# Optimization experiments

Measured on AMD Instinct MI355X. Metric: run time of the kernel, lower is better.

Reference implementation:

```python
import jax, jax.numpy as jnp
import numpy as np

B, N, D = 8, 2048, 768
H = 12
HD = D // H
W = 16          # window_size
HOP = 8         # hop_size
GB = N // 2 + 1   # global freq bins = 1025
LB = W // 2 + 1   # local freq bins = 9
NW = (N - W) // HOP + 1  # num windows = 255
EPS_LN = 1e-5


def setup_inputs() -> dict:
    key = jax.random.key(0)
    ks = jax.random.split(key, 12)
    s = 0.02
    return {
        "x": jax.random.normal(ks[0], (B, N, D), dtype=jnp.float32),
        "base_filter_global": jnp.ones((H, GB, 1), jnp.float32),
        "base_filter_local": jnp.ones((H, LB, 1), jnp.float32),
        "modrelu_bias_global": jnp.full((H, GB, 1), -0.1, jnp.float32),
        "modrelu_bias_local": jnp.full((H, LB, 1), -0.1, jnp.float32),
        "w1g": jax.random.normal(ks[1], (D, D), jnp.float32) * s,
        "b1g": jnp.zeros((D,), jnp.float32),
        "w2g": jax.random.normal(ks[2], (D, H * GB), jnp.float32) * s,
        "b2g": jnp.zeros((H * GB,), jnp.float32),
        "w1l": jax.random.normal(ks[3], (D, D), jnp.float32) * s,
        "b1l": jnp.zeros((D,), jnp.float32),
        "w2l": jax.random.normal(ks[4], (D, H * LB), jnp.float32) * s,
        "b2l": jnp.zeros((H * LB,), jnp.float32),
        "fusion_w": jax.random.normal(ks[5], (2,), jnp.float32) * 0.5,
        "ln_gamma": jnp.ones((D,), jnp.float32),
        "ln_beta": jnp.zeros((D,), jnp.float32),
    }


def _modrelu(z, bias):
    # modReLU: ReLU(|z| + b) * z / |z|  (|z| clamped at 1e-6 in denominator)
    a = jnp.abs(z)
    return z * (jax.nn.relu(a + bias) / jnp.maximum(a, 1e-6))


def _hann(w):
    # torch.hann_window default (periodic=True)
    n = jnp.arange(w, dtype=jnp.float32)
    return 0.5 * (1.0 - jnp.cos(2.0 * jnp.pi * n / w))


def reference(x, base_filter_global, base_filter_local, modrelu_bias_global,
              modrelu_bias_local, w1g, b1g, w2g, b2g, w1l, b1l, w2l, b2l,
              fusion_w, ln_gamma, ln_beta):
    b, n, d = x.shape
    x_heads = x.reshape(b, n, H, HD).transpose(0, 2, 1, 3)  # (B,H,N,hd)

    # ---- global branch ----
    Fg = jnp.fft.rfft(x_heads, axis=2, norm='ortho')  # (B,H,GB,hd) complex
    ctx = x.mean(axis=1)  # (B,D)
    mg = jnp.tanh(jax.nn.gelu(ctx @ w1g + b1g, approximate=False) @ w2g + b2g)
    mg = mg.reshape(b, H, GB, 1)
    Fg = Fg * (base_filter_global[None] + mg)
    Fg = _modrelu(Fg, modrelu_bias_global[None])
    x_global = jnp.fft.irfft(Fg, n=n, axis=2, norm='ortho')  # (B,H,N,hd)

    # ---- local (STFT) branch ----
    idx = jnp.arange(NW)[:, None] * HOP + jnp.arange(W)[None, :]  # (NW,W)
    x_win = x_heads[:, :, idx, :]  # (B,H,NW,W,hd)
    w = _hann(W)[None, None, None, :, None]
    x_win = x_win * w
    Fl = jnp.fft.rfft(x_win, axis=3, norm='ortho')  # (B,H,NW,LB,hd)
    ml = jnp.tanh(jax.nn.gelu(ctx @ w1l + b1l, approximate=False) @ w2l + b2l)
    ml = ml.reshape(b, H, 1, LB, 1)
    Fl = Fl * (base_filter_local[None, :, None] + ml)
    Fl = _modrelu(Fl, modrelu_bias_local[None, :, None])
    x_lwin = jnp.fft.irfft(Fl, n=W, axis=3, norm='ortho') * w  # (B,H,NW,W,hd)

    # vectorized overlap-add
    flat_idx = idx.reshape(-1)  # (NW*W,)
    x_local = jnp.zeros((b, H, n, HD), x.dtype).at[:, :, flat_idx, :].add(
        x_lwin.reshape(b, H, NW * W, HD))

    # ---- fuse + residual + layernorm ----
    fused = x_global * fusion_w[0] + x_local * fusion_w[1]  # Linear(2,1,bias=False)
    x_out = fused.transpose(0, 2, 1, 3).reshape(b, n, d)
    y = x + x_out  # dropout is identity at p=0 / eval
    mu = y.mean(axis=-1, keepdims=True)
    var = y.var(axis=-1, keepdims=True)
    return (y - mu) / jnp.sqrt(var + EPS_LN) * ln_gamma + ln_beta
```

## Files before the change

### kernel.cpp

```cpp
#include <hip/hip_runtime.h>
#include <math.h>

#define B_  8
#define N_  2048
#define D_  768
#define H_  12
#define HD_ 64
#define GB_ 1025
#define LB_ 9
#define NW_ 255

#define CBX(i) ((i) + ((i) >> 4))

#define C1_ 0.92387953251128674f
#define S1_ 0.38268343236508978f
#define R2_ 0.70710678118654752f

#define FBF(i,k,wr,wi) { const float ar=yr[i],ai=yi[i],br=yr[k],bi=yi[k]; \
  yr[i]=ar+br; yi[i]=ai+bi; const float dr=ar-br, di=ai-bi; \
  yr[k]=fmaf(dr,wr,-(di*(wi))); yi[k]=fmaf(dr,wi,di*(wr)); }
#define FBF1(i,k) { const float ar=yr[i],ai=yi[i],br=yr[k],bi=yi[k]; \
  yr[i]=ar+br; yi[i]=ai+bi; yr[k]=ar-br; yi[k]=ai-bi; }
#define FBFmi(i,k) { const float ar=yr[i],ai=yi[i],br=yr[k],bi=yi[k]; \
  yr[i]=ar+br; yi[i]=ai+bi; yr[k]=ai-bi; yi[k]=br-ar; }

#define IBF(i,k,wr,wi) { const float br=yr[k],bi=yi[k]; \
  const float tr=fmaf(br,wr,-(bi*(wi))), ti=fmaf(br,wi,bi*(wr)); \
  yr[k]=yr[i]-tr; yi[k]=yi[i]-ti; yr[i]+=tr; yi[i]+=ti; }
#define IBF1(i,k) { const float tr=yr[k], ti=yi[k]; \
  yr[k]=yr[i]-tr; yi[k]=yi[i]-ti; yr[i]+=tr; yi[i]+=ti; }
#define IBFpi(i,k) { const float tr=-yi[k], ti=yr[k]; \
  yr[k]=yr[i]-tr; yi[k]=yi[i]-ti; yr[i]+=tr; yi[i]+=ti; }

__device__ __forceinline__ float2 cmulf(float2 a, float2 b) {
  return make_float2(fmaf(a.x, b.x, -(a.y*b.y)), fmaf(a.x, b.y, a.y*b.x));
}
__device__ __forceinline__ float2 caddf(float2 a, float2 b){ return make_float2(a.x+b.x, a.y+b.y); }
__device__ __forceinline__ float2 csubf(float2 a, float2 b){ return make_float2(a.x-b.x, a.y-b.y); }

__global__ __launch_bounds__(256) void k_ctx(const float* __restrict__ x,
                                             float* __restrict__ ctx) {
  const int b = blockIdx.x;
  const int nc = blockIdx.y;
  const int tid = threadIdx.x;
  const int n0 = nc * 64;
  for (int c = tid; c < D_; c += 256) {
    float s = 0.0f;
    #pragma unroll 4
    for (int n = 0; n < 64; ++n)
      s += x[((size_t)(b*N_ + n0 + n))*D_ + c];
    atomicAdd(&ctx[b*D_ + c], s);
  }
}

__global__ __launch_bounds__(256) void k_mlp1(
    const float* __restrict__ ctx,
    const float* __restrict__ w1g, const float* __restrict__ b1g,
    const float* __restrict__ w1l, const float* __restrict__ b1l,
    float* __restrict__ h1g, float* __restrict__ h1l) {
  __shared__ float hs[B_*D_];
  __shared__ float red[4][16][33];
  const int tid = threadIdx.x;
  const bool isl = (blockIdx.y != 0);
  const float* w1 = isl ? w1l : w1g;
  const float* b1 = isl ? b1l : b1g;
  float*       h1 = isl ? h1l : h1g;
  const int j0 = (int)blockIdx.x * 64;

  for (int i = tid; i < B_*D_; i += 256) hs[i] = ctx[i] * (1.0f/(float)N_);
  __syncthreads();

  const int jg    = tid & 15;
  const int slice = tid >> 4;
  const int j     = j0 + jg*4;
  float acc[8][4] = {};
  {
    const float4* w14 = (const float4*)w1;
    const int jc = j >> 2;
    const int i0 = slice*48;
    #pragma unroll 4
    for (int ii = 0; ii < 48; ++ii) {
      const int i = i0 + ii;
      const float4 w = w14[(size_t)i*192 + jc];
      #pragma unroll
      for (int b = 0; b < 8; ++b) {
        const float hv = hs[b*D_ + i];
        acc[b][0] = fmaf(hv, w.x, acc[b][0]);
        acc[b][1] = fmaf(hv, w.y, acc[b][1]);
        acc[b][2] = fmaf(hv, w.z, acc[b][2]);
        acc[b][3] = fmaf(hv, w.w, acc[b][3]);
      }
    }
  }
  #pragma unroll
  for (int b = 0; b < 8; ++b) {
    #pragma unroll
    for (int q = 0; q < 4; ++q) {
      float v = acc[b][q];
      v += __shfl_xor(v, 16, 64);
      v += __shfl_xor(v, 32, 64);
      acc[b][q] = v;
    }
  }
  const int wv = tid >> 6;
  if ((tid & 63) < 16) {
    #pragma unroll
    for (int b = 0; b < 8; ++b)
      #pragma unroll
      for (int q = 0; q < 4; ++q)
        red[wv][jg][b*4+q] = acc[b][q];
  }
  __syncthreads();
  for (int s = tid; s < 512; s += 256) {
    const int jg2 = s >> 5;
    const int v2  = s & 31;
    const int b   = v2 >> 2, q = v2 & 3;
    const int jo  = j0 + jg2*4 + q;
    const float sum = red[0][jg2][v2] + red[1][jg2][v2]
                    + red[2][jg2][v2] + red[3][jg2][v2];
    const float v = sum + b1[jo];
    h1[(size_t)b*D_ + jo] = 0.5f * v * (1.0f + erff(v * 0.70710678118654752f));
  }
}

__global__ __launch_bounds__(256) void k_mlp2(
    const float* __restrict__ h1g, const float* __restrict__ h1l,
    const float* __restrict__ w2g, const float* __restrict__ b2g,
    const float* __restrict__ w2l, const float* __restrict__ b2l,
    float* __restrict__ mg, float* __restrict__ ml) {
  __shared__ float hs[B_*D_];
  __shared__ float red[4][16][33];
  const int tid = threadIdx.x;
  const bool isg = (blockIdx.x < 193);
  const float* h1 = isg ? h1g : h1l;
  const float* w2 = isg ? w2g : w2l;
  const float* b2 = isg ? b2g : b2l;
  float*       mo = isg ? mg  : ml;
  const int Jmax = isg ? (H_*GB_) : (H_*LB_);
  const int j0   = isg ? (int)blockIdx.x*64 : ((int)blockIdx.x-193)*64;

  for (int i = tid; i < B_*D_; i += 256) hs[i] = h1[i];
  __syncthreads();

  const int jg    = tid & 15;
  const int slice = tid >> 4;
  const int j     = j0 + jg*4;
  float acc[8][4] = {};
  if (j < Jmax) {
    const float4* w24 = (const float4*)w2;
    const int jc   = j >> 2;
    const int rowq = Jmax >> 2;
    const int i0   = slice*48;
    #pragma unroll 4
    for (int ii = 0; ii < 48; ++ii) {
      const int i = i0 + ii;
      const float4 w = w24[(size_t)i*rowq + jc];
      #pragma unroll
      for (int b = 0; b < 8; ++b) {
        const float hv = hs[b*D_ + i];
        acc[b][0] = fmaf(hv, w.x, acc[b][0]);
        acc[b][1] = fmaf(hv, w.y, acc[b][1]);
        acc[b][2] = fmaf(hv, w.z, acc[b][2]);
        acc[b][3] = fmaf(hv, w.w, acc[b][3]);
      }
    }
  }
  #pragma unroll
  for (int b = 0; b < 8; ++b) {
    #pragma unroll
    for (int q = 0; q < 4; ++q) {
      float v = acc[b][q];
      v += __shfl_xor(v, 16, 64);
      v += __shfl_xor(v, 32, 64);
      acc[b][q] = v;
    }
  }
  const int wv = tid >> 6;
  if ((tid & 63) < 16) {
    #pragma unroll
    for (int b = 0; b < 8; ++b)
      #pragma unroll
      for (int q = 0; q < 4; ++q)
        red[wv][jg][b*4+q] = acc[b][q];
  }
  __syncthreads();
  for (int s = tid; s < 512; s += 256) {
    const int jg2 = s >> 5;
    const int v2  = s & 31;
    const int b   = v2 >> 2, q = v2 & 3;
    const int jo  = j0 + jg2*4 + q;
    if (jo < Jmax) {
      const float sum = red[0][jg2][v2] + red[1][jg2][v2]
                      + red[2][jg2][v2] + red[3][jg2][v2];
      mo[(size_t)b*Jmax + jo] = tanhf(sum + b2[jo]);
    }
  }
}

__global__ __launch_bounds__(256) void k_spectral(
    const float* __restrict__ x,
    const float* __restrict__ bfg, const float* __restrict__ bfl,
    const float* __restrict__ mbg, const float* __restrict__ mbl,
    const float* __restrict__ mg,  const float* __restrict__ ml,
    const float* __restrict__ fw,  float* __restrict__ fused) {
  __shared__ float2 cb[N_ + (N_>>4)];
  __shared__ float2 tw[1024];
  __shared__ float  t1b[4][8], t2b[4][8];
  __shared__ float  lf[LB_], lb[LB_];

  const int tid = threadIdx.x;
  const int id  = blockIdx.x;
  const int v_  = (id & 7) * 384 + (id >> 3);
  const int dp  = v_ & 31;
  const int bh  = v_ >> 5;
  const int h   = bh % H_;
  const int b   = bh / H_;
  const int d   = dp * 2;
  const int c   = h*HD_ + d;
  const int col0 = bh*HD_ + d;

  for (int m = tid; m < 1024; m += 256) {
    float s_, c_;
    sincospif(-(float)m * (1.0f/1024.0f), &s_, &c_);
    tw[m] = make_float2(c_, s_);
  }
  if (tid < LB_) {
    lf[tid] = bfl[h*LB_ + tid] + ml[(size_t)b*(H_*LB_) + h*LB_ + tid];
    lb[tid] = mbl[h*LB_ + tid];
  }
  for (int n = tid; n < N_; n += 256) {
    const float2 v = *(const float2*)&x[((size_t)(b*N_ + n))*D_ + c];
    cb[CBX(n)] = v;
  }
  __syncthreads();

  const float HWIN[16] = {0.0f, 0.038060233744356624f, 0.14644660940672624f, 0.30865828381745508f,
                          0.5f, 0.69134171618254492f, 0.85355339059327376f, 0.96193976625564337f,
                          1.0f, 0.96193976625564337f, 0.85355339059327376f, 0.69134171618254492f,
                          0.5f, 0.30865828381745508f, 0.14644660940672624f, 0.038060233744356624f};
  float w1a[16], w2a[16];
  {
    const int j = tid;
    if (j < NW_) {
      float yr[16], yi[16];
      #pragma unroll
      for (int t = 0; t < 16; ++t) {
        const float2 v = cb[CBX(j*8 + t)];
        yr[t] = v.x * HWIN[t];
        yi[t] = v.y * HWIN[t];
      }
      FBF1(0,8); FBF(1,9,C1_,-S1_); FBF(2,10,R2_,-R2_); FBF(3,11,S1_,-C1_);
      FBFmi(4,12); FBF(5,13,-S1_,-C1_); FBF(6,14,-R2_,-R2_); FBF(7,15,-C1_,-S1_);
      FBF1(0,4); FBF(1,5,R2_,-R2_); FBFmi(2,6); FBF(3,7,-R2_,-R2_);
      FBF1(8,12); FBF(9,13,R2_,-R2_); FBFmi(10,14); FBF(11,15,-R2_,-R2_);
      FBF1(0,2); FBFmi(1,3); FBF1(4,6); FBFmi(5,7);
      FBF1(8,10); FBFmi(9,11); FBF1(12,14); FBFmi(13,15);
      FBF1(0,1); FBF1(2,3); FBF1(4,5); FBF1(6,7);
      FBF1(8,9); FBF1(10,11); FBF1(12,13); FBF1(14,15);
      {
        const int IA[9] = {0,8,4,12,2,10,6,14,1};
        const int IB[9] = {0,15,7,11,3,13,5,9,1};
        #pragma unroll
        for (int l = 0; l <= 8; ++l) {
          const int ia = IA[l], ib = IB[l];
          const float Zar=yr[ia], Zai=yi[ia], Zbr=yr[ib], Zbi=yi[ib];
          float f1r = 0.125f*(Zar+Zbr), f1i = 0.125f*(Zai-Zbi);
          float f2r = 0.125f*(Zai+Zbi), f2i = 0.125f*(Zbr-Zar);
          const float ft = lf[l], bs = lb[l];
          f1r *= ft; f1i *= ft; f2r *= ft; f2i *= ft;
          const float a1 = sqrtf(f1r*f1r + f1i*f1i);
          const float m1 = fmaxf(a1 + bs, 0.0f) / fmaxf(a1, 1e-6f);
          f1r *= m1; f1i *= m1;
          const float a2 = sqrtf(f2r*f2r + f2i*f2i);
          const float m2 = fmaxf(a2 + bs, 0.0f) / fmaxf(a2, 1e-6f);
          f2r *= m2; f2i *= m2;
          yr[ia] = f1r - f2i; yi[ia] = f1i + f2r;
          if (l >= 1 && l <= 7) { yr[ib] = f1r + f2i; yi[ib] = f2r - f1i; }
        }
      }
      IBF1(0,1); IBF1(2,3); IBF1(4,5); IBF1(6,7);
      IBF1(8,9); IBF1(10,11); IBF1(12,13); IBF1(14,15);
      IBF1(0,2); IBFpi(1,3); IBF1(4,6); IBFpi(5,7);
      IBF1(8,10); IBFpi(9,11); IBF1(12,14); IBFpi(13,15);
      IBF1(0,4); IBF(1,5,R2_,R2_); IBFpi(2,6); IBF(3,7,-R2_,R2_);
      IBF1(8,12); IBF(9,13,R2_,R2_); IBFpi(10,14); IBF(11,15,-R2_,R2_);
      IBF1(0,8); IBF(1,9,C1_,S1_); IBF(2,10,R2_,R2_); IBF(3,11,S1_,C1_);
      IBFpi(4,12); IBF(5,13,-S1_,C1_); IBF(6,14,-R2_,R2_); IBF(7,15,-C1_,S1_);
      #pragma unroll
      for (int t = 0; t < 16; ++t) {
        const float q = 0.25f * HWIN[t];
        w1a[t] = yr[t] * q;
        w2a[t] = yi[t] * q;
      }
    } else {
      #pragma unroll
      for (int t = 0; t < 16; ++t) { w1a[t] = 0.0f; w2a[t] = 0.0f; }
    }
  }
  const int lane = tid & 63, wvi = tid >> 6;
  if (lane == 63 && tid < NW_) {
    #pragma unroll
    for (int s = 0; s < 8; ++s) { t1b[wvi][s] = w1a[8+s]; t2b[wvi][s] = w2a[8+s]; }
  }
  __syncthreads();

  float r1[8], r2[8];
  #pragma unroll
  for (int s = 0; s < 8; ++s) {
    float p1 = __shfl_up(w1a[s+8], 1, 64);
    float p2 = __shfl_up(w2a[s+8], 1, 64);
    if (lane == 0) {
      p1 = wvi ? t1b[wvi-1][s] : 0.0f;
      p2 = wvi ? t2b[wvi-1][s] : 0.0f;
    }
    r1[s] = w1a[s] + p1;
    r2[s] = w2a[s] + p2;
  }

  #pragma unroll
  for (int sh = 10; sh >= 2; sh -= 2) {
    const int hspan = 1 << sh, hh = hspan >> 1;
    for (int t = tid; t < 512; t += 256) {
      const int p  = t & (hh-1);
      const int g  = t >> (sh-1);
      const int i0 = (g << (sh+1)) | p;
      float2 a = cb[CBX(i0)], bb = cb[CBX(i0+hh)], cc = cb[CBX(i0+hspan)], dd = cb[CBX(i0+hspan+hh)];
      const float2 w1  = tw[p << (10-sh)];
      const float2 w1b = tw[(p+hh) << (10-sh)];
      const float2 w2  = tw[p << (11-sh)];
      float2 ap = caddf(a, cc),  cp = cmulf(csubf(a, cc), w1);
      float2 bp = caddf(bb, dd), dp2 = cmulf(csubf(bb, dd), w1b);
      cb[CBX(i0)]          = caddf(ap, bp);
      cb[CBX(i0+hh)]       = cmulf(csubf(ap, bp), w2);
      cb[CBX(i0+hspan)]    = caddf(cp, dp2);
      cb[CBX(i0+hspan+hh)] = cmulf(csubf(cp, dp2), w2);
    }
    __syncthreads();
  }
  for (int t = tid; t < 1024; t += 256) {
    const int i0 = t << 1;
    float2 a = cb[CBX(i0)], bb = cb[CBX(i0+1)];
    cb[CBX(i0)]   = caddf(a, bb);
    cb[CBX(i0+1)] = csubf(a, bb);
  }
  __syncthreads();

  const float fsc = 0.022097086912079610f;
  {
    const float* mgp = mg + (size_t)b*(H_*GB_) + h*GB_;
    const float* bfp = bfg + h*GB_;
    const float* mbp = mbg + h*GB_;
    for (int k = tid; k < 1024; k += 256) {
      if (k == 0) {
        float2 Z0 = cb[CBX(0)], Zn = cb[CBX(1)];
        float g1 = Z0.x * fsc, g2 = Z0.y * fsc;
        {
          const float filt = bfp[0] + mgp[0], bias = mbp[0];
          g1 *= filt; g2 *= filt;
          float a1 = fabsf(g1); g1 *= fmaxf(a1 + bias, 0.0f) / fmaxf(a1, 1e-6f);
          float a2 = fabsf(g2); g2 *= fmaxf(a2 + bias, 0.0f) / fmaxf(a2, 1e-6f);
        }
        cb[CBX(0)] = make_float2(g1, g2);
        float n1 = Zn.x * fsc, n2 = Zn.y * fsc;
        {
          const float filt = bfp[1024] + mgp[1024], bias = mbp[1024];
          n1 *= filt; n2 *= filt;
          float a1 = fabsf(n1); n1 *= fmaxf(a1 + bias, 0.0f) / fmaxf(a1, 1e-6f);
          float a2 = fabsf(n2); n2 *= fmaxf(a2 + bias, 0.0f) / fmaxf(a2, 1e-6f);
        }
        cb[CBX(1)] = make_float2(n1, n2);
      } else {
        const int ik  = (int)(__brev((unsigned)k) >> 21);
        const int imk = (int)(__brev((unsigned)(2048 - k)) >> 21);
        const float2 Za = cb[CBX(ik)], Zb = cb[CBX(imk)];
        const float hs_ = 0.5f * fsc;
        float f1r = (Za.x + Zb.x) * hs_, f1i = (Za.y - Zb.y) * hs_;
        float f2r = (Za.y + Zb.y) * hs_, f2i = (Zb.x - Za.x) * hs_;
        const float filt = bfp[k] + mgp[k], bias = mbp[k];
        f1r *= filt; f1i *= filt; f2r *= filt; f2i *= filt;
        const float a1 = sqrtf(f1r*f1r + f1i*f1i);
        const float s1 = fmaxf(a1 + bias, 0.0f) / fmaxf(a1, 1e-6f);
        f1r *= s1; f1i *= s1;
        const float a2 = sqrtf(f2r*f2r + f2i*f2i);
        const float s2 = fmaxf(a2 + bias, 0.0f) / fmaxf(a2, 1e-6f);
        f2r *= s2; f2i *= s2;
        cb[CBX(ik)]  = make_float2(f1r - f2i, f1i + f2r);
        cb[CBX(imk)] = make_float2(f1r + f2i, f2r - f1i);
      }
    }
  }
  __syncthreads();

  for (int t = tid; t < 1024; t += 256) {
    const int i0 = t << 1;
    float2 a = cb[CBX(i0)], bb = cb[CBX(i0+1)];
    cb[CBX(i0)]   = caddf(a, bb);
    cb[CBX(i0+1)] = csubf(a, bb);
  }
  __syncthreads();
  #pragma unroll
  for (int sh = 2; sh <= 10; sh += 2) {
    const int hspan = 1 << sh, hh = hspan >> 1;
    for (int t = tid; t < 512; t += 256) {
      const int p  = t & (hh-1);
      const int g  = t >> (sh-1);
      const int i0 = (g << (sh+1)) | p;
      float2 a = cb[CBX(i0)], bb = cb[CBX(i0+hh)], cc = cb[CBX(i0+hspan)], dd = cb[CBX(i0+hspan+hh)];
      float2 w2  = tw[p << (11-sh)];       w2.y  = -w2.y;
      float2 w1  = tw[p << (10-sh)];       w1.y  = -w1.y;
      float2 w1b = tw[(p+hh) << (10-sh)];  w1b.y = -w1b.y;
      float2 t1 = cmulf(bb, w2);
      float2 ap = caddf(a, t1),  bp = csubf(a, t1);
      float2 t2 = cmulf(dd, w2);
      float2 cp = caddf(cc, t2), dp2 = csubf(cc, t2);
      float2 T = cmulf(cp, w1);
      float2 U = cmulf(dp2, w1b);
      cb[CBX(i0)]          = caddf(ap, T);
      cb[CBX(i0+hspan)]    = csubf(ap, T);
      cb[CBX(i0+hh)]       = caddf(bp, U);
      cb[CBX(i0+hspan+hh)] = csubf(bp, U);
    }
    __syncthreads();
  }

  const float fw1v = fw[1];
  const float fwg  = fw[0] * fsc;
  float* f0 = fused + (size_t)col0 * N_;
  float* f1p = f0 + N_;
  const int n0 = tid * 8;
  float v0[8], v1[8];
  #pragma unroll
  for (int s = 0; s < 8; ++s) {
    const float2 g = cb[CBX(n0 + s)];
    v0[s] = fwg * g.x + fw1v * r1[s];
    v1[s] = fwg * g.y + fw1v * r2[s];
  }
  *(float4*)&f0[n0]    = make_float4(v0[0], v0[1], v0[2], v0[3]);
  *(float4*)&f0[n0+4]  = make_float4(v0[4], v0[5], v0[6], v0[7]);
  *(float4*)&f1p[n0]   = make_float4(v1[0], v1[1], v1[2], v1[3]);
  *(float4*)&f1p[n0+4] = make_float4(v1[4], v1[5], v1[6], v1[7]);
}

__global__ __launch_bounds__(256) void k_ln(const float* __restrict__ x,
                                            const float* __restrict__ fused,
                                            const float* __restrict__ gamma,
                                            const float* __restrict__ beta,
                                            float* __restrict__ out) {
  __shared__ float yt[16*776];
  __shared__ float mus[16], rsd[16];
  const int bi = blockIdx.x;
  const int b  = bi >> 7;
  const int n0 = (bi & 127) * 16;
  const int tid = threadIdx.x;

  {
    const float4* x4 = (const float4*)(x + ((size_t)(b*N_ + n0))*D_);
    for (int i = tid; i < 16*D_/4; i += 256) {
      const int nn = i / 192, r = i - nn*192;
      const float4 v = x4[i];
      float* yp = &yt[nn*776 + r*4];
      yp[0] = v.x; yp[1] = v.y; yp[2] = v.z; yp[3] = v.w;
    }
  }
  __syncthreads();
  {
    const float4* fu4 = (const float4*)fused;
    for (int i = tid; i < 16*D_/4; i += 256) {
      const int cc = i >> 2, q = (i & 3) * 4;
      const float4 g = fu4[(((size_t)(b*D_ + cc))*N_ + n0)/4 + (i & 3)];
      yt[(q+0)*776 + cc] += g.x;
      yt[(q+1)*776 + cc] += g.y;
      yt[(q+2)*776 + cc] += g.z;
      yt[(q+3)*776 + cc] += g.w;
    }
  }
  __syncthreads();
  const int nn = tid >> 4, cl = tid & 15;
  float s1 = 0.0f, s2 = 0.0f;
  for (int c = cl; c < D_; c += 16) {
    const float v = yt[nn*776 + c];
    s1 += v; s2 += v*v;
  }
  #pragma unroll
  for (int m = 8; m >= 1; m >>= 1) {
    s1 += __shfl_xor(s1, m, 16);
    s2 += __shfl_xor(s2, m, 16);
  }
  if (cl == 0) {
    const float mu  = s1 * (1.0f/(float)D_);
    const float var = s2 * (1.0f/(float)D_) - mu*mu;
    mus[nn] = mu;
    rsd[nn] = rsqrtf(var + 1e-5f);
  }
  __syncthreads();
  {
    float4* o4 = (float4*)(out + ((size_t)(b*N_ + n0))*D_);
    const float4* g4 = (const float4*)gamma;
    const float4* be4 = (const float4*)beta;
    for (int i = tid; i < 16*D_/4; i += 256) {
      const int nn2 = i / 192, r = i - nn2*192;
      const float mu = mus[nn2], rs = rsd[nn2];
      const float4 gm = g4[r], bt = be4[r];
      const float* yp = &yt[nn2*776 + r*4];
      float4 o;
      o.x = (yp[0] - mu) * rs * gm.x + bt.x;
      o.y = (yp[1] - mu) * rs * gm.y + bt.y;
      o.z = (yp[2] - mu) * rs * gm.z + bt.z;
      o.w = (yp[3] - mu) * rs * gm.w + bt.w;
      o4[i] = o;
    }
  }
}

extern "C" void kernel_launch(void* const* d_in, const int* in_sizes, int n_in,
                              void* d_out, int out_size, void* d_ws, size_t ws_size,
                              hipStream_t stream) {
  const float* x   = (const float*)d_in[0];
  const float* bfg = (const float*)d_in[1];
  const float* bfl = (const float*)d_in[2];
  const float* mbg = (const float*)d_in[3];
  const float* mbl = (const float*)d_in[4];
  const float* w1g = (const float*)d_in[5];
  const float* b1g = (const float*)d_in[6];
  const float* w2g = (const float*)d_in[7];
  const float* b2g = (const float*)d_in[8];
  const float* w1l = (const float*)d_in[9];
  const float* b1l = (const float*)d_in[10];
  const float* w2l = (const float*)d_in[11];
  const float* b2l = (const float*)d_in[12];
  const float* fw  = (const float*)d_in[13];
  const float* gam = (const float*)d_in[14];
  const float* bet = (const float*)d_in[15];
  float* out = (float*)d_out;

  float* ws    = (float*)d_ws;
  float* ctx   = ws;
  float* h1g   = ws + 6144;
  float* h1l   = ws + 12288;
  float* mg    = ws + 18432;
  float* ml    = ws + 116832;
  float* fused = ws + 117696;

  hipMemsetAsync(ctx, 0, (size_t)B_*D_*sizeof(float), stream);
  k_ctx<<<dim3(B_, 32), 256, 0, stream>>>(x, ctx);
  k_mlp1<<<dim3(12, 2), 256, 0, stream>>>(ctx, w1g, b1g, w1l, b1l, h1g, h1l);
  k_mlp2<<<195, 256, 0, stream>>>(h1g, h1l, w2g, b2g, w2l, b2l, mg, ml);
  k_spectral<<<B_*H_*32, 256, 0, stream>>>(x, bfg, bfl, mbg, mbl, mg, ml, fw, fused);
  k_ln<<<B_*N_/16, 256, 0, stream>>>(x, fused, gam, bet, out);
}
```

Before: 312.2 us.

## Restructure 2048-point shared-memory FFT into radix-8 passes with derived twiddles

Replaces the radix-4 plus final radix-2 shared-memory FFT (six passes, each followed by a barrier, both forward and inverse) with four radix-8-style passes of 8 points per thread. Higher-power twiddles are derived in registers by squaring the base twiddle, so the twiddle table shrinks from 1024 to 256 padded entries and fewer sincos calls are needed. This aims to cut LDS round-trips and __syncthreads barriers. The cost is more registers per thread and a small extra rounding error from the squared twiddles.

```diff
diff --git a/kernel.cpp b/kernel.cpp
--- a/kernel.cpp
+++ b/kernel.cpp
@@ -11,6 +11,7 @@
 #define NW_ 255
 
 #define CBX(i) ((i) + ((i) >> 4))
+#define TWX(i) ((i) + ((i) >> 4))
 
 #define C1_ 0.92387953251128674f
 #define S1_ 0.38268343236508978f
@@ -35,8 +36,133 @@
 __device__ __forceinline__ float2 cmulf(float2 a, float2 b) {
   return make_float2(fmaf(a.x, b.x, -(a.y*b.y)), fmaf(a.x, b.y, a.y*b.x));
 }
+__device__ __forceinline__ float2 cmulcf(float2 a, float2 b) {
+  return make_float2(fmaf(a.x, b.x, a.y*b.y), fmaf(a.y, b.x, -(a.x*b.y)));
+}
 __device__ __forceinline__ float2 caddf(float2 a, float2 b){ return make_float2(a.x+b.x, a.y+b.y); }
 __device__ __forceinline__ float2 csubf(float2 a, float2 b){ return make_float2(a.x-b.x, a.y-b.y); }
+__device__ __forceinline__ float2 csqf(float2 a){ return make_float2(fmaf(a.x,a.x,-(a.y*a.y)), 2.0f*a.x*a.y); }
+
+template<int S, int L>
+__device__ __forceinline__ void fft_trip_fwd(float2* cb, const float2* tw, int j) {
+  const int r    = j & (S-1);
+  const int base = r + ((j >> L) << (L+3));
+  float2 v[8];
+  #pragma unroll
+  for (int k = 0; k < 8; ++k) v[k] = cb[CBX(base + S*k)];
+  const float2 w = tw[TWX(r * (256/S))];
+  const float2 c8 = make_float2(R2_, -R2_);
+  float2 W1[4];
+  W1[0] = w;
+  W1[1] = cmulf(w, c8);
+  W1[2] = make_float2(w.y, -w.x);
+  W1[3] = make_float2(W1[1].y, -W1[1].x);
+  #pragma unroll
+  for (int k = 0; k < 4; ++k) {
+    const float2 u = v[k], t = v[k+4];
+    v[k]   = caddf(u, t);
+    v[k+4] = cmulf(csubf(u, t), W1[k]);
+  }
+  const float2 w2  = csqf(w);
+  const float2 w2i = make_float2(w2.y, -w2.x);
+  {
+    float2 d;
+    d = csubf(v[0], v[2]); v[0] = caddf(v[0], v[2]); v[2] = cmulf(d, w2);
+    d = csubf(v[1], v[3]); v[1] = caddf(v[1], v[3]); v[3] = cmulf(d, w2i);
+    d = csubf(v[4], v[6]); v[4] = caddf(v[4], v[6]); v[6] = cmulf(d, w2);
+    d = csubf(v[5], v[7]); v[5] = caddf(v[5], v[7]); v[7] = cmulf(d, w2i);
+  }
+  const float2 w4 = csqf(w2);
+  #pragma unroll
+  for (int k = 0; k < 8; k += 2) {
+    const float2 d = csubf(v[k], v[k+1]);
+    v[k]   = caddf(v[k], v[k+1]);
+    v[k+1] = cmulf(d, w4);
+  }
+  #pragma unroll
+  for (int k = 0; k < 8; ++k) cb[CBX(base + S*k)] = v[k];
+}
+
+__device__ __forceinline__ void fft_trip4_fwd(float2* cb, int j) {
+  const int base = j << 3;
+  float2 v[8];
+  #pragma unroll
+  for (int k = 0; k < 8; ++k) v[k] = cb[CBX(base + k)];
+  float2 d;
+  d = csubf(v[0], v[2]); v[0] = caddf(v[0], v[2]); v[2] = d;
+  d = csubf(v[1], v[3]); v[1] = caddf(v[1], v[3]); v[3] = make_float2(d.y, -d.x);
+  d = csubf(v[4], v[6]); v[4] = caddf(v[4], v[6]); v[6] = d;
+  d = csubf(v[5], v[7]); v[5] = caddf(v[5], v[7]); v[7] = make_float2(d.y, -d.x);
+  #pragma unroll
+  for (int k = 0; k < 8; k += 2) {
+    d = csubf(v[k], v[k+1]);
+    v[k]   = caddf(v[k], v[k+1]);
+    v[k+1] = d;
+  }
+  #pragma unroll
+  for (int k = 0; k < 8; ++k) cb[CBX(base + k)] = v[k];
+}
+
+__device__ __forceinline__ void fft_trip1_inv(float2* cb, int j) {
+  const int base = j << 3;
+  float2 v[8];
+  #pragma unroll
+  for (int k = 0; k < 8; ++k) v[k] = cb[CBX(base + k)];
+  #pragma unroll
+  for (int k = 0; k < 8; k += 2) {
+    const float2 t = v[k+1];
+    v[k+1] = csubf(v[k], t);
+    v[k]   = caddf(v[k], t);
+  }
+  {
+    float2 t;
+    t = v[2];                              v[2] = csubf(v[0], t); v[0] = caddf(v[0], t);
+    t = make_float2(-v[3].y, v[3].x);      v[3] = csubf(v[1], t); v[1] = caddf(v[1], t);
+    t = v[6];                              v[6] = csubf(v[4], t); v[4] = caddf(v[4], t);
+    t = make_float2(-v[7].y, v[7].x);      v[7] = csubf(v[5], t); v[5] = caddf(v[5], t);
+  }
+  #pragma unroll
+  for (int k = 0; k < 8; ++k) cb[CBX(base + k)] = v[k];
+}
+
+template<int S, int L>
+__device__ __forceinline__ void fft_trip_inv(float2* cb, const float2* tw, int j) {
+  const int r    = j & (S-1);
+  const int base = r + ((j >> L) << (L+3));
+  float2 v[8];
+  #pragma unroll
+  for (int k = 0; k < 8; ++k) v[k] = cb[CBX(base + S*k)];
+  const float2 w  = tw[TWX(r * (256/S))];
+  const float2 w2 = csqf(w);
+  const float2 w4 = csqf(w2);
+  #pragma unroll
+  for (int k = 0; k < 8; k += 2) {
+    const float2 t = cmulcf(v[k+1], w4);
+    v[k+1] = csubf(v[k], t);
+    v[k]   = caddf(v[k], t);
+  }
+  {
+    float2 t;
+    t = cmulcf(v[2], w2);                          v[2] = csubf(v[0], t); v[0] = caddf(v[0], t);
+    t = cmulcf(v[3], w2); t = make_float2(-t.y, t.x); v[3] = csubf(v[1], t); v[1] = caddf(v[1], t);
+    t = cmulcf(v[6], w2);                          v[6] = csubf(v[4], t); v[4] = caddf(v[4], t);
+    t = cmulcf(v[7], w2); t = make_float2(-t.y, t.x); v[7] = csubf(v[5], t); v[5] = caddf(v[5], t);
+  }
+  const float2 c8 = make_float2(R2_, -R2_);
+  float2 W1[4];
+  W1[0] = w;
+  W1[1] = cmulf(w, c8);
+  W1[2] = make_float2(w.y, -w.x);
+  W1[3] = make_float2(W1[1].y, -W1[1].x);
+  #pragma unroll
+  for (int k = 0; k < 4; ++k) {
+    const float2 t = cmulcf(v[k+4], W1[k]);
+    v[k+4] = csubf(v[k], t);
+    v[k]   = caddf(v[k], t);
+  }
+  #pragma unroll
+  for (int k = 0; k < 8; ++k) cb[CBX(base + S*k)] = v[k];
+}
 
 __global__ __launch_bounds__(256) void k_ctx(const float* __restrict__ x,
                                              float* __restrict__ ctx) {
@@ -204,7 +330,7 @@
     const float* __restrict__ mg,  const float* __restrict__ ml,
     const float* __restrict__ fw,  float* __restrict__ fused) {
   __shared__ float2 cb[N_ + (N_>>4)];
-  __shared__ float2 tw[1024];
+  __shared__ float2 tw[256 + 16];
   __shared__ float  t1b[4][8], t2b[4][8];
   __shared__ float  lf[LB_], lb[LB_];
 
@@ -219,10 +345,10 @@
   const int c   = h*HD_ + d;
   const int col0 = bh*HD_ + d;
 
-  for (int m = tid; m < 1024; m += 256) {
+  {
     float s_, c_;
-    sincospif(-(float)m * (1.0f/1024.0f), &s_, &c_);
-    tw[m] = make_float2(c_, s_);
+    sincospif(-(float)tid * (1.0f/1024.0f), &s_, &c_);
+    tw[TWX(tid)] = make_float2(c_, s_);
   }
   if (tid < LB_) {
     lf[tid] = bfl[h*LB_ + tid] + ml[(size_t)b*(H_*LB_) + h*LB_ + tid];
@@ -317,33 +443,10 @@
     r2[s] = w2a[s] + p2;
   }
 
-  #pragma unroll
-  for (int sh = 10; sh >= 2; sh -= 2) {
-    const int hspan = 1 << sh, hh = hspan >> 1;
-    for (int t = tid; t < 512; t += 256) {
-      const int p  = t & (hh-1);
-      const int g  = t >> (sh-1);
-      const int i0 = (g << (sh+1)) | p;
-      float2 a = cb[CBX(i0)], bb = cb[CBX(i0+hh)], cc = cb[CBX(i0+hspan)], dd = cb[CBX(i0+hspan+hh)];
-      const float2 w1  = tw[p << (10-sh)];
-      const float2 w1b = tw[(p+hh) << (10-sh)];
-      const float2 w2  = tw[p << (11-sh)];
-      float2 ap = caddf(a, cc),  cp = cmulf(csubf(a, cc), w1);
-      float2 bp = caddf(bb, dd), dp2 = cmulf(csubf(bb, dd), w1b);
-      cb[CBX(i0)]          = caddf(ap, bp);
-      cb[CBX(i0+hh)]       = cmulf(csubf(ap, bp), w2);
-      cb[CBX(i0+hspan)]    = caddf(cp, dp2);
-      cb[CBX(i0+hspan+hh)] = cmulf(csubf(cp, dp2), w2);
-    }
-    __syncthreads();
-  }
-  for (int t = tid; t < 1024; t += 256) {
-    const int i0 = t << 1;
-    float2 a = cb[CBX(i0)], bb = cb[CBX(i0+1)];
-    cb[CBX(i0)]   = caddf(a, bb);
-    cb[CBX(i0+1)] = csubf(a, bb);
-  }
-  __syncthreads();
+  fft_trip_fwd<256,8>(cb, tw, tid); __syncthreads();
+  fft_trip_fwd< 32,5>(cb, tw, tid); __syncthreads();
+  fft_trip_fwd<  4,2>(cb, tw, tid); __syncthreads();
+  fft_trip4_fwd(cb, tid);           __syncthreads();
 
   const float fsc = 0.022097086912079610f;
   {
@@ -391,37 +494,10 @@
   }
   __syncthreads();
 
-  for (int t = tid; t < 1024; t += 256) {
-    const int i0 = t << 1;
-    float2 a = cb[CBX(i0)], bb = cb[CBX(i0+1)];
-    cb[CBX(i0)]   = caddf(a, bb);
-    cb[CBX(i0+1)] = csubf(a, bb);
-  }
-  __syncthreads();
-  #pragma unroll
-  for (int sh = 2; sh <= 10; sh += 2) {
-    const int hspan = 1 << sh, hh = hspan >> 1;
-    for (int t = tid; t < 512; t += 256) {
-      const int p  = t & (hh-1);
-      const int g  = t >> (sh-1);
-      const int i0 = (g << (sh+1)) | p;
-      float2 a = cb[CBX(i0)], bb = cb[CBX(i0+hh)], cc = cb[CBX(i0+hspan)], dd = cb[CBX(i0+hspan+hh)];
-      float2 w2  = tw[p << (11-sh)];       w2.y  = -w2.y;
-      float2 w1  = tw[p << (10-sh)];       w1.y  = -w1.y;
-      float2 w1b = tw[(p+hh) << (10-sh)];  w1b.y = -w1b.y;
-      float2 t1 = cmulf(bb, w2);
-      float2 ap = caddf(a, t1),  bp = csubf(a, t1);
-      float2 t2 = cmulf(dd, w2);
-      float2 cp = caddf(cc, t2), dp2 = csubf(cc, t2);
-      float2 T = cmulf(cp, w1);
-      float2 U = cmulf(dp2, w1b);
-      cb[CBX(i0)]          = caddf(ap, T);
-      cb[CBX(i0+hspan)]    = csubf(ap, T);
-      cb[CBX(i0+hh)]       = caddf(bp, U);
-      cb[CBX(i0+hspan+hh)] = csubf(bp, U);
-    }
-    __syncthreads();
-  }
+  fft_trip1_inv(cb, tid);           __syncthreads();
+  fft_trip_inv<  4,2>(cb, tw, tid); __syncthreads();
+  fft_trip_inv< 32,5>(cb, tw, tid); __syncthreads();
+  fft_trip_inv<256,8>(cb, tw, tid); __syncthreads();
 
   const float fw1v = fw[1];
   const float fwg  = fw[0] * fsc;
```

After: 297.7 us. -4.6%, faster.
